# Performance work log

Measured on AMD Instinct MI355X. Metric: run time of the kernel, lower is better.

## Reference

```python
import jax, jax.numpy as jnp
import numpy as np

N = 50000          # total nodes (1000 graphs x 50 agents)
E = 800000         # edges
B = 1000           # batch of graphs -> one agent node each
IN_DIM = 64
HID = 32           # hidden_dim == TransformerConv out_channels per head
HEADS = 4
OUT_DIM = 5
FINAL = HID + HID * HEADS * 2  # 288


def _tconv(x, src, dst, wq, bq, wk, bk, wv, bv):
    """PyG TransformerConv, root_weight=False, concat=True, no edge_attr."""
    n = x.shape[0]
    q = (x @ wq + bq).reshape(n, HEADS, HID)
    k = (x @ wk + bk).reshape(n, HEADS, HID)
    v = (x @ wv + bv).reshape(n, HEADS, HID)
    # per-edge attention logits: query at target, key at source
    alpha = jnp.sum(q[dst] * k[src], axis=-1) / jnp.sqrt(jnp.float32(HID))  # [E, HEADS]
    # segment softmax over incoming edges of each target node
    amax = jax.lax.stop_gradient(jax.ops.segment_max(alpha, dst, num_segments=n))
    ex = jnp.exp(alpha - amax[dst])
    denom = jax.ops.segment_sum(ex, dst, num_segments=n)
    attn = ex / (denom[dst] + 1e-16)                                        # [E, HEADS]
    out = jax.ops.segment_sum(v[src] * attn[..., None], dst, num_segments=n)
    return out.reshape(n, HEADS * HID)


def setup_inputs() -> dict:
    key = jax.random.key(0)
    ks = jax.random.split(key, 24)
    g = lambda i, shape, fan: (jax.random.normal(ks[i], shape, jnp.float32)
                               / jnp.sqrt(jnp.float32(fan)))
    d1 = HID * HEADS  # conv1 output width / conv2 input width
    inp = {
        "x": jax.random.normal(ks[0], (N, IN_DIM), jnp.float32),
        "edge_index": jax.random.randint(ks[1], (2, E), 0, N, jnp.int64),
        "dm_mask": (jax.random.uniform(ks[2], (N, 1)) > 0.5).astype(jnp.float32),
        "global_indices": jax.random.randint(ks[3], (B,), 0, N, jnp.int64),
        # encoder MLP: in -> hid (relu) -> hid
        "enc_w1": g(4, (IN_DIM, HID), IN_DIM), "enc_b1": jnp.zeros((HID,), jnp.float32),
        "enc_w2": g(5, (HID, HID), HID),       "enc_b2": jnp.zeros((HID,), jnp.float32),
        # conv1: hid -> heads*hid
        "c1_wq": g(6, (HID, d1), HID), "c1_bq": jnp.zeros((d1,), jnp.float32),
        "c1_wk": g(7, (HID, d1), HID), "c1_bk": jnp.zeros((d1,), jnp.float32),
        "c1_wv": g(8, (HID, d1), HID), "c1_bv": jnp.zeros((d1,), jnp.float32),
        # conv2: heads*hid -> heads*hid
        "c2_wq": g(9, (d1, d1), d1),  "c2_bq": jnp.zeros((d1,), jnp.float32),
        "c2_wk": g(10, (d1, d1), d1), "c2_bk": jnp.zeros((d1,), jnp.float32),
        "c2_wv": g(11, (d1, d1), d1), "c2_bv": jnp.zeros((d1,), jnp.float32),
        # output head
        "out_w": g(12, (FINAL, OUT_DIM), FINAL),
        "out_b": jnp.zeros((OUT_DIM,), jnp.float32),
    }
    return inp


def reference(x, edge_index, dm_mask, global_indices,
              enc_w1, enc_b1, enc_w2, enc_b2,
              c1_wq, c1_bq, c1_wk, c1_bk, c1_wv, c1_bv,
              c2_wq, c2_bq, c2_wk, c2_bk, c2_wv, c2_bv,
              out_w, out_b):
    src, dst = edge_index[0], edge_index[1]
    # encoder MLP + relu (forward applies F.relu on encoder output)
    h = jax.nn.relu(x @ enc_w1 + enc_b1)
    h = jax.nn.relu(h @ enc_w2 + enc_b2)            # [N, HID]
    x1 = h[global_indices]                          # [B, HID]
    h = jax.nn.relu(_tconv(h, src, dst, c1_wq, c1_bq, c1_wk, c1_bk, c1_wv, c1_bv))
    x2 = h[global_indices]                          # [B, HEADS*HID]
    h = h * dm_mask                                 # decision-maker masking
    h = jax.nn.relu(_tconv(h, src, dst, c2_wq, c2_bq, c2_wk, c2_bk, c2_wv, c2_bv))
    x3 = h[global_indices]                          # [B, HEADS*HID]
    x_cat = jnp.concatenate([x1, x2, x3], axis=1)   # [B, FINAL]
    return x_cat @ out_w + out_b                    # [B, OUT_DIM]
```

## Files before the change

kernel.cpp:

```cpp
#include <hip/hip_runtime.h>
#include <math.h>


typedef _Float16 half8 __attribute__((ext_vector_type(8)));
typedef float f32x4 __attribute__((ext_vector_type(4)));

__device__ inline half8 h8zero() {
    half8 r;
#pragma unroll
    for (int j = 0; j < 8; ++j) r[j] = (_Float16)0.f;
    return r;
}

__device__ __forceinline__ void enc_body(const float* __restrict__ x,
                                         const float* __restrict__ w1, const float* __restrict__ b1,
                                         const float* __restrict__ w2, const float* __restrict__ b2,
                                         _Float16* __restrict__ h0, int n, int bn,
                                         float* __restrict__ smem) {
    float* W1s = smem;
    float* W2s = smem + 2048;
    float* B1s = smem + 3072;
    float* B2s = smem + 3104;
    float* xs  = smem + 3136;
    float* hs  = smem + 3648;
    int t = threadIdx.x;
    for (int i = t; i < 64 * 32; i += 256) W1s[i] = w1[i];
    for (int i = t; i < 32 * 32; i += 256) W2s[i] = w2[i];
    if (t < 32) { B1s[t] = b1[t]; B2s[t] = b2[t]; }
    if (t < 128) {
        int row = t >> 4;
        float4 val = make_float4(0.f, 0.f, 0.f, 0.f);
        if (bn + row < n) val = *(const float4*)(x + (size_t)bn * 64 + t * 4);
        ((float4*)xs)[t] = val;
    }
    __syncthreads();
    int nn = t >> 5, c = t & 31;
    float acc = B1s[c];
#pragma unroll
    for (int i = 0; i < 64; ++i) acc += xs[nn * 64 + i] * W1s[i * 32 + c];
    acc = fmaxf(acc, 0.f);
    hs[nn * 32 + c] = acc;
    __syncthreads();
    float acc2 = B2s[c];
#pragma unroll
    for (int i = 0; i < 32; ++i) acc2 += hs[nn * 32 + i] * W2s[i * 32 + c];
    acc2 = fmaxf(acc2, 0.f);
    int node = bn + nn;
    if (node < n) h0[(size_t)node * 32 + c] = (_Float16)acc2;
}

__global__ __launch_bounds__(256)
void prep_kernel(const float* __restrict__ x,
                 const float* __restrict__ ew1, const float* __restrict__ eb1,
                 const float* __restrict__ ew2, const float* __restrict__ eb2,
                 _Float16* __restrict__ h0,
                 const float* __restrict__ q1, const float* __restrict__ k1,
                 const float* __restrict__ v1, _Float16* __restrict__ WT1,
                 const float* __restrict__ q2, const float* __restrict__ k2,
                 const float* __restrict__ v2, _Float16* __restrict__ WT2,
                 const int* __restrict__ dstv, int* __restrict__ deg, int* __restrict__ eslot,
                 int n, int e, int wtb, int histb) {
    __shared__ float smem[3904];
    int b = blockIdx.x, t = threadIdx.x;
    if (b < wtb) {
        int tid = b * 256 + t;
        const int n1 = 3 * 128 * 32;
        if (tid < n1) {
            int z = tid / (128 * 32);
            int rem = tid % (128 * 32);
            int c = rem / 32, k = rem % 32;
            const float* w = (z == 0) ? q1 : ((z == 1) ? k1 : v1);
            WT1[tid] = (_Float16)w[k * 128 + c];
        } else {
            int i = tid - n1;
            if (i < 3 * 128 * 128) {
                int z = i / (128 * 128);
                int rem = i % (128 * 128);
                int c = rem / 128, k = rem % 128;
                const float* w = (z == 0) ? q2 : ((z == 1) ? k2 : v2);
                WT2[i] = (_Float16)w[k * 128 + c];
            }
        }
    } else if (b < wtb + histb) {
        int i = (b - wtb) * 256 + t;
        if (i < e) eslot[i] = atomicAdd(&deg[dstv[i]], 1);
    } else {
        enc_body(x, ew1, eb1, ew2, eb2, h0, n, (b - wtb - histb) * 8, smem);
    }
}

__device__ __forceinline__ void qkv_body(const _Float16* __restrict__ X, const float* __restrict__ mask,
                                         const _Float16* __restrict__ WT,
                                         const float* __restrict__ Bq, const float* __restrict__ Bk,
                                         const float* __restrict__ Bv,
                                         _Float16* __restrict__ Q, _Float16* __restrict__ KV,
                                         int n, int IN, int bx, int z,
                                         _Float16* __restrict__ Xs, _Float16* __restrict__ Ws) {
    int t = threadIdx.x;
    int bm = bx * 64;
    const float* Bz = (z == 0) ? Bq : ((z == 1) ? Bk : Bv);
    _Float16* Y;
    size_t ystride;
    if (z == 0) { Y = Q; ystride = 128; }
    else        { Y = KV + (z == 1 ? 0 : 128); ystride = 256; }

    int lane = t & 63, w = t >> 6;
    int wr = w >> 1, wc = w & 1;
    int fr = lane & 15, k0 = (lane >> 4) * 8;
    f32x4 acc[2][4];
#pragma unroll
    for (int i = 0; i < 2; ++i)
#pragma unroll
        for (int j = 0; j < 4; ++j)
#pragma unroll
            for (int r = 0; r < 4; ++r) acc[i][j][r] = 0.f;

    int srow = t >> 2, sseg = (t & 3) * 8;
    int snode = bm + srow;
    const _Float16* xbase = X + (size_t)snode * IN + sseg;
    const _Float16* wbase = WT + (size_t)(z * 128) * IN + sseg;
    bool xvalid = (snode < n);
    if (xvalid && mask) xvalid = (mask[snode] != 0.f);

    for (int kt = 0; kt < IN; kt += 32) {
        half8 xv = h8zero();
        if (xvalid) xv = *(const half8*)(xbase + kt);
        half8 wv0 = *(const half8*)(wbase + (size_t)srow * IN + kt);
        half8 wv1 = *(const half8*)(wbase + (size_t)(64 + srow) * IN + kt);
        __syncthreads();
        *(half8*)&Xs[srow * 40 + sseg] = xv;
        *(half8*)&Ws[srow * 40 + sseg] = wv0;
        *(half8*)&Ws[(64 + srow) * 40 + sseg] = wv1;
        __syncthreads();
        half8 a0 = *(const half8*)&Xs[(wr * 32 + fr) * 40 + k0];
        half8 a1 = *(const half8*)&Xs[(wr * 32 + 16 + fr) * 40 + k0];
#pragma unroll
        for (int tc = 0; tc < 4; ++tc) {
            half8 bfr = *(const half8*)&Ws[(wc * 64 + tc * 16 + fr) * 40 + k0];
            acc[0][tc] = __builtin_amdgcn_mfma_f32_16x16x32_f16(a0, bfr, acc[0][tc], 0, 0, 0);
            acc[1][tc] = __builtin_amdgcn_mfma_f32_16x16x32_f16(a1, bfr, acc[1][tc], 0, 0, 0);
        }
    }
#pragma unroll
    for (int tc = 0; tc < 4; ++tc) {
        int colc = wc * 64 + tc * 16 + fr;
        float bias = Bz[colc];
#pragma unroll
        for (int tr = 0; tr < 2; ++tr) {
#pragma unroll
            for (int reg = 0; reg < 4; ++reg) {
                int node = bm + wr * 32 + tr * 16 + (lane >> 4) * 4 + reg;
                if (node < n) Y[(size_t)node * ystride + colc] = (_Float16)(acc[tr][tc][reg] + bias);
            }
        }
    }
}

__global__ __launch_bounds__(256)
void scan1_qkv1_kernel(const int* __restrict__ deg, int* __restrict__ rp,
                       int* __restrict__ bsum, int n, int nb,
                       const _Float16* __restrict__ h0, const _Float16* __restrict__ WT1,
                       const float* __restrict__ bq, const float* __restrict__ bk,
                       const float* __restrict__ bv,
                       _Float16* __restrict__ Q, _Float16* __restrict__ KV, int nqx) {
    __shared__ _Float16 sm[64 * 40 + 128 * 40];
    int b = blockIdx.x;
    if (b < nb) {
        int* s = (int*)sm;
        int t = threadIdx.x;
        int gid = b * 256 + t;
        int v = (gid < n) ? deg[gid] : 0;
        s[t] = v;
        __syncthreads();
#pragma unroll
        for (int off = 1; off < 256; off <<= 1) {
            int tv = (t >= off) ? s[t - off] : 0;
            __syncthreads();
            s[t] += tv;
            __syncthreads();
        }
        if (gid < n) rp[gid] = s[t] - v;
        if (t == 255) bsum[b] = s[255];
    } else {
        int r = b - nb;
        int z = r / nqx, bx = r % nqx;
        qkv_body(h0, nullptr, WT1, bq, bk, bv, Q, KV, n, 32, bx, z, sm, sm + 64 * 40);
    }
}

__global__ __launch_bounds__(256)
void qkv2_kernel(const _Float16* __restrict__ X, const float* __restrict__ mask,
                 const _Float16* __restrict__ WT,
                 const float* __restrict__ Bq, const float* __restrict__ Bk,
                 const float* __restrict__ Bv,
                 _Float16* __restrict__ Q, _Float16* __restrict__ KV, int n, int IN) {
    __shared__ _Float16 Xs[64 * 40];
    __shared__ _Float16 Ws[128 * 40];
    qkv_body(X, mask, WT, Bq, Bk, Bv, Q, KV, n, IN, blockIdx.x, blockIdx.y, Xs, Ws);
}

__global__ void scan2_kernel(int* bsum, int nb) {
    __shared__ int s[256];
    int t = threadIdx.x;
    int v = (t < nb) ? bsum[t] : 0;
    s[t] = v;
    __syncthreads();
#pragma unroll
    for (int off = 1; off < 256; off <<= 1) {
        int tv = (t >= off) ? s[t - off] : 0;
        __syncthreads();
        s[t] += tv;
        __syncthreads();
    }
    if (t < nb) bsum[t] = s[t] - v;
}
__global__ void scan3_kernel(int* rp, const int* __restrict__ bsum, int n) {
    int gid = blockIdx.x * 256 + threadIdx.x;
    if (gid < n) rp[gid] += bsum[blockIdx.x];
}
__global__ void scatter_kernel(const int* __restrict__ src, const int* __restrict__ dst,
                               const int* __restrict__ rp, const int* __restrict__ eslot,
                               int* __restrict__ col, int e) {
    int i = blockIdx.x * 256 + threadIdx.x;
    if (i < e) col[rp[dst[i]] + eslot[i]] = src[i];
}

__global__ __launch_bounds__(256)
void attn_kernel(const _Float16* __restrict__ q, const _Float16* __restrict__ kv,
                 const int* __restrict__ rp, const int* __restrict__ deg,
                 const int* __restrict__ col,
                 _Float16* __restrict__ out, int n) {
    int w = threadIdx.x >> 6;
    int lane = threadIdx.x & 63;
    int node = blockIdx.x * 4 + w;
    if (node >= n) return;
    int es = lane >> 4;
    int l = lane & 15;
    int d0 = l * 8;
    float qf[8];
    {
        half8 qh = *(const half8*)(q + (size_t)node * 128 + d0);
#pragma unroll
        for (int j = 0; j < 8; ++j) qf[j] = (float)qh[j];
    }
    int start = rp[node], len = deg[node];
    float s = 0.f;
    float acc[8];
#pragma unroll
    for (int j = 0; j < 8; ++j) acc[j] = 0.f;
    const float sc = 0.17677669529663689f * 1.4426950408889634f;

    for (int i = es; i < len; i += 4) {
        int srcn = col[start + i];
        const _Float16* row = kv + (size_t)srcn * 256 + d0;
        half8 kf = *(const half8*)row;
        float dot = 0.f;
#pragma unroll
        for (int j = 0; j < 8; ++j) dot += qf[j] * (float)kf[j];
        dot += __shfl_xor(dot, 1);
        dot += __shfl_xor(dot, 2);
        float a = fminf(fmaxf(dot * sc, -120.f), 120.f);
        float p = __builtin_amdgcn_exp2f(a);
        half8 vf = *(const half8*)(row + 128);
        s += p;
#pragma unroll
        for (int j = 0; j < 8; ++j) acc[j] += p * (float)vf[j];
    }
#pragma unroll
    for (int half = 16; half <= 32; half <<= 1) {
        s += __shfl_xor(s, half);
#pragma unroll
        for (int j = 0; j < 8; ++j) acc[j] += __shfl_xor(acc[j], half);
    }
    if (es == 0) {
        float inv = 1.f / (s + 1e-16f);
        half8 r;
#pragma unroll
        for (int j = 0; j < 8; ++j) r[j] = (_Float16)fmaxf(acc[j] * inv, 0.f);
        *(half8*)(out + (size_t)node * 128 + d0) = r;
    }
}

__global__ void head_kernel(const _Float16* __restrict__ h0, const _Float16* __restrict__ h1,
                            const _Float16* __restrict__ h2, const int* __restrict__ gi,
                            const float* __restrict__ ow, const float* __restrict__ ob,
                            float* __restrict__ out, int bsz) {
    int idx = blockIdx.x * 256 + threadIdx.x;
    if (idx >= bsz * 5) return;
    int b = idx / 5, c = idx % 5;
    int g = gi[b];
    float acc = ob[c];
    const _Float16* r0 = h0 + (size_t)g * 32;
#pragma unroll
    for (int i = 0; i < 32; ++i) acc += (float)r0[i] * ow[i * 5 + c];
    const _Float16* r1 = h1 + (size_t)g * 128;
#pragma unroll
    for (int i = 0; i < 128; ++i) acc += (float)r1[i] * ow[(32 + i) * 5 + c];
    const _Float16* r2 = h2 + (size_t)g * 128;
#pragma unroll
    for (int i = 0; i < 128; ++i) acc += (float)r2[i] * ow[(160 + i) * 5 + c];
    out[idx] = acc;
}

extern "C" void kernel_launch(void* const* d_in, const int* in_sizes, int n_in,
                              void* d_out, int out_size, void* d_ws, size_t ws_size,
                              hipStream_t stream) {
    const float* x    = (const float*)d_in[0];
    const int*   ei   = (const int*)d_in[1];
    const float* dm   = (const float*)d_in[2];
    const int*   gi   = (const int*)d_in[3];
    const float* ew1  = (const float*)d_in[4];
    const float* eb1  = (const float*)d_in[5];
    const float* ew2  = (const float*)d_in[6];
    const float* eb2  = (const float*)d_in[7];
    const float* c1wq = (const float*)d_in[8];
    const float* c1bq = (const float*)d_in[9];
    const float* c1wk = (const float*)d_in[10];
    const float* c1bk = (const float*)d_in[11];
    const float* c1wv = (const float*)d_in[12];
    const float* c1bv = (const float*)d_in[13];
    const float* c2wq = (const float*)d_in[14];
    const float* c2bq = (const float*)d_in[15];
    const float* c2wk = (const float*)d_in[16];
    const float* c2bk = (const float*)d_in[17];
    const float* c2wv = (const float*)d_in[18];
    const float* c2bv = (const float*)d_in[19];
    const float* ow   = (const float*)d_in[20];
    const float* ob   = (const float*)d_in[21];
    float* out = (float*)d_out;

    int N = in_sizes[0] / 64;
    int E = in_sizes[1] / 2;
    int B = in_sizes[3];
    const int* srcv = ei;
    const int* dstv = ei + E;

    char* ws = (char*)d_ws;
    size_t off = 0;
    auto alloc = [&](size_t bytes) -> void* {
        void* p = ws + off;
        off += (bytes + 255) & ~(size_t)255;
        return p;
    };
    _Float16* h0   = (_Float16*)alloc((size_t)N * 32 * 2);
    _Float16* h1   = (_Float16*)alloc((size_t)N * 128 * 2);
    _Float16* h2   = (_Float16*)alloc((size_t)N * 128 * 2);
    _Float16* Q    = (_Float16*)alloc((size_t)N * 128 * 2);
    _Float16* KV   = (_Float16*)alloc((size_t)N * 256 * 2);
    _Float16* WT1  = (_Float16*)alloc((size_t)3 * 128 * 32 * 2);
    _Float16* WT2  = (_Float16*)alloc((size_t)3 * 128 * 128 * 2);
    int* deg   = (int*)alloc((size_t)N * 4);
    int* rp    = (int*)alloc((size_t)N * 4);
    int* eslot = (int*)alloc((size_t)E * 4);
    int* colb  = (int*)alloc((size_t)E * 4);
    int* bsum  = (int*)alloc(4096);

    hipMemsetAsync(deg, 0, (size_t)N * 4, stream);

    int eb = (E + 255) / 256;
    int nb = (N + 255) / 256;
    int nqx = (N + 63) / 64;
    int wtb = (3 * 128 * 32 + 3 * 128 * 128 + 255) / 256;

    prep_kernel<<<wtb + eb + (N + 7) / 8, 256, 0, stream>>>(
        x, ew1, eb1, ew2, eb2, h0,
        c1wq, c1wk, c1wv, WT1, c2wq, c2wk, c2wv, WT2,
        dstv, deg, eslot, N, E, wtb, eb);

    scan1_qkv1_kernel<<<nb + 3 * nqx, 256, 0, stream>>>(
        deg, rp, bsum, N, nb, h0, WT1, c1bq, c1bk, c1bv, Q, KV, nqx);

    scan2_kernel<<<1, 256, 0, stream>>>(bsum, nb);
    scan3_kernel<<<nb, 256, 0, stream>>>(rp, bsum, N);
    scatter_kernel<<<eb, 256, 0, stream>>>(srcv, dstv, rp, eslot, colb, E);

    attn_kernel<<<(N + 3) / 4, 256, 0, stream>>>(Q, KV, rp, deg, colb, h1, N);

    dim3 gq(nqx, 3);
    qkv2_kernel<<<gq, 256, 0, stream>>>(h1, dm, WT2, c2bq, c2bk, c2bv, Q, KV, N, 128);
    attn_kernel<<<(N + 3) / 4, 256, 0, stream>>>(Q, KV, rp, deg, colb, h2, N);

    head_kernel<<<(B * 5 + 255) / 256, 256, 0, stream>>>(h0, h1, h2, gi, ow, ob, out, B);
}
```

Baseline: 244.9 us.

## Replace CSR scan with atomic segment allocation and restructure attention edge parallelism

```diff
diff --git a/kernel.cpp b/kernel.cpp
--- a/kernel.cpp
+++ b/kernel.cpp
@@ -3,6 +3,7 @@
 
 
 typedef _Float16 half8 __attribute__((ext_vector_type(8)));
+typedef _Float16 half2t __attribute__((ext_vector_type(2)));
 typedef float f32x4 __attribute__((ext_vector_type(4)));
 
 __device__ inline half8 h8zero() {
@@ -10,6 +11,22 @@
 #pragma unroll
     for (int j = 0; j < 8; ++j) r[j] = (_Float16)0.f;
     return r;
+}
+
+__device__ __forceinline__ float dot8(half8 a, half8 b, float c) {
+#if __has_builtin(__builtin_amdgcn_fdot2)
+#pragma unroll
+    for (int j = 0; j < 4; ++j) {
+        half2t x, y;
+        x[0] = a[2 * j]; x[1] = a[2 * j + 1];
+        y[0] = b[2 * j]; y[1] = b[2 * j + 1];
+        c = __builtin_amdgcn_fdot2(x, y, c, false);
+    }
+#else
+#pragma unroll
+    for (int j = 0; j < 8; ++j) c += (float)a[j] * (float)b[j];
+#endif
+    return c;
 }
 
 __device__ __forceinline__ void enc_body(const float* __restrict__ x,
@@ -157,32 +174,31 @@
 }
 
 __global__ __launch_bounds__(256)
-void scan1_qkv1_kernel(const int* __restrict__ deg, int* __restrict__ rp,
-                       int* __restrict__ bsum, int n, int nb,
+void alloc_qkv1_kernel(const int* __restrict__ deg, int* __restrict__ rp,
+                       int* __restrict__ cnt, int n, int nab,
                        const _Float16* __restrict__ h0, const _Float16* __restrict__ WT1,
                        const float* __restrict__ bq, const float* __restrict__ bk,
                        const float* __restrict__ bv,
                        _Float16* __restrict__ Q, _Float16* __restrict__ KV, int nqx) {
     __shared__ _Float16 sm[64 * 40 + 128 * 40];
     int b = blockIdx.x;
-    if (b < nb) {
-        int* s = (int*)sm;
-        int t = threadIdx.x;
+    if (b < nab) {
+        int t = threadIdx.x, lane = t & 63;
         int gid = b * 256 + t;
         int v = (gid < n) ? deg[gid] : 0;
-        s[t] = v;
-        __syncthreads();
-#pragma unroll
-        for (int off = 1; off < 256; off <<= 1) {
-            int tv = (t >= off) ? s[t - off] : 0;
-            __syncthreads();
-            s[t] += tv;
-            __syncthreads();
-        }
-        if (gid < n) rp[gid] = s[t] - v;
-        if (t == 255) bsum[b] = s[255];
+        int incl = v;
+#pragma unroll
+        for (int off = 1; off < 64; off <<= 1) {
+            int tv = __shfl_up(incl, off);
+            if (lane >= off) incl += tv;
+        }
+        int tot = __shfl(incl, 63);
+        int base = 0;
+        if (lane == 0 && tot > 0) base = atomicAdd(cnt, tot);
+        base = __shfl(base, 0);
+        if (gid < n) rp[gid] = base + incl - v;
     } else {
-        int r = b - nb;
+        int r = b - nab;
         int z = r / nqx, bx = r % nqx;
         qkv_body(h0, nullptr, WT1, bq, bk, bv, Q, KV, n, 32, bx, z, sm, sm + 64 * 40);
     }
@@ -199,25 +215,6 @@
     qkv_body(X, mask, WT, Bq, Bk, Bv, Q, KV, n, IN, blockIdx.x, blockIdx.y, Xs, Ws);
 }
 
-__global__ void scan2_kernel(int* bsum, int nb) {
-    __shared__ int s[256];
-    int t = threadIdx.x;
-    int v = (t < nb) ? bsum[t] : 0;
-    s[t] = v;
-    __syncthreads();
-#pragma unroll
-    for (int off = 1; off < 256; off <<= 1) {
-        int tv = (t >= off) ? s[t - off] : 0;
-        __syncthreads();
-        s[t] += tv;
-        __syncthreads();
-    }
-    if (t < nb) bsum[t] = s[t] - v;
-}
-__global__ void scan3_kernel(int* rp, const int* __restrict__ bsum, int n) {
-    int gid = blockIdx.x * 256 + threadIdx.x;
-    if (gid < n) rp[gid] += bsum[blockIdx.x];
-}
 __global__ void scatter_kernel(const int* __restrict__ src, const int* __restrict__ dst,
                                const int* __restrict__ rp, const int* __restrict__ eslot,
                                int* __restrict__ col, int e) {
@@ -234,15 +231,18 @@
     int lane = threadIdx.x & 63;
     int node = blockIdx.x * 4 + w;
     if (node >= n) return;
-    int es = lane >> 4;
-    int l = lane & 15;
-    int d0 = l * 8;
-    float qf[8];
-    {
-        half8 qh = *(const half8*)(q + (size_t)node * 128 + d0);
-#pragma unroll
-        for (int j = 0; j < 8; ++j) qf[j] = (float)qh[j];
-    }
+    int eo  = lane >> 2;
+    int hq  = lane & 3;
+    int dl  = lane & 15;
+    int sub = lane >> 4;
+    int hd  = dl >> 2;
+
+    const _Float16* qp = q + (size_t)node * 128 + hq * 32;
+    half8 q0 = *(const half8*)(qp);
+    half8 q1 = *(const half8*)(qp + 8);
+    half8 q2 = *(const half8*)(qp + 16);
+    half8 q3 = *(const half8*)(qp + 24);
+
     int start = rp[node], len = deg[node];
     float s = 0.f;
     float acc[8];
@@ -250,34 +250,46 @@
     for (int j = 0; j < 8; ++j) acc[j] = 0.f;
     const float sc = 0.17677669529663689f * 1.4426950408889634f;
 
-    for (int i = es; i < len; i += 4) {
-        int srcn = col[start + i];
-        const _Float16* row = kv + (size_t)srcn * 256 + d0;
-        half8 kf = *(const half8*)row;
+    for (int base = 0; base < len; base += 16) {
+        int rem = len - base;
+        int i = base + eo;
+        bool valid = (i < len);
+        int srcn = valid ? col[start + i] : 0;
+        const _Float16* kp = kv + (size_t)srcn * 256 + hq * 32;
+        half8 k0 = *(const half8*)(kp);
+        half8 k1 = *(const half8*)(kp + 8);
+        half8 k2 = *(const half8*)(kp + 16);
+        half8 k3 = *(const half8*)(kp + 24);
         float dot = 0.f;
-#pragma unroll
-        for (int j = 0; j < 8; ++j) dot += qf[j] * (float)kf[j];
-        dot += __shfl_xor(dot, 1);
-        dot += __shfl_xor(dot, 2);
+        dot = dot8(q0, k0, dot);
+        dot = dot8(q1, k1, dot);
+        dot = dot8(q2, k2, dot);
+        dot = dot8(q3, k3, dot);
         float a = fminf(fmaxf(dot * sc, -120.f), 120.f);
-        float p = __builtin_amdgcn_exp2f(a);
-        half8 vf = *(const half8*)(row + 128);
-        s += p;
-#pragma unroll
-        for (int j = 0; j < 8; ++j) acc[j] += p * (float)vf[j];
-    }
-#pragma unroll
-    for (int half = 16; half <= 32; half <<= 1) {
-        s += __shfl_xor(s, half);
-#pragma unroll
-        for (int j = 0; j < 8; ++j) acc[j] += __shfl_xor(acc[j], half);
-    }
-    if (es == 0) {
+        float p = valid ? __builtin_amdgcn_exp2f(a) : 0.f;
+        int ng = (rem >= 16) ? 4 : ((rem + 3) >> 2);
+        for (int g = 0; g < ng; ++g) {
+            int e = g * 4 + sub;
+            float pj = __shfl(p, e * 4 + hd);
+            int   sj = __shfl(srcn, e * 4);
+            half8 vf = *(const half8*)(kv + (size_t)sj * 256 + 128 + dl * 8);
+            s += pj;
+#pragma unroll
+            for (int j = 0; j < 8; ++j) acc[j] += pj * (float)vf[j];
+        }
+    }
+#pragma unroll
+    for (int mask = 16; mask <= 32; mask <<= 1) {
+        s += __shfl_xor(s, mask);
+#pragma unroll
+        for (int j = 0; j < 8; ++j) acc[j] += __shfl_xor(acc[j], mask);
+    }
+    if (sub == 0) {
         float inv = 1.f / (s + 1e-16f);
         half8 r;
 #pragma unroll
         for (int j = 0; j < 8; ++j) r[j] = (_Float16)fmaxf(acc[j] * inv, 0.f);
-        *(half8*)(out + (size_t)node * 128 + d0) = r;
+        *(half8*)(out + (size_t)node * 128 + dl * 8) = r;
     }
 }
 
@@ -349,16 +361,16 @@
     _Float16* KV   = (_Float16*)alloc((size_t)N * 256 * 2);
     _Float16* WT1  = (_Float16*)alloc((size_t)3 * 128 * 32 * 2);
     _Float16* WT2  = (_Float16*)alloc((size_t)3 * 128 * 128 * 2);
+    int* cnt   = (int*)alloc(256);
     int* deg   = (int*)alloc((size_t)N * 4);
     int* rp    = (int*)alloc((size_t)N * 4);
     int* eslot = (int*)alloc((size_t)E * 4);
     int* colb  = (int*)alloc((size_t)E * 4);
-    int* bsum  = (int*)alloc(4096);
-
-    hipMemsetAsync(deg, 0, (size_t)N * 4, stream);
-
-    int eb = (E + 255) / 256;
-    int nb = (N + 255) / 256;
+
+    hipMemsetAsync(cnt, 0, 256 + (size_t)N * 4, stream);
+
+    int eb  = (E + 255) / 256;
+    int nab = (N + 255) / 256;
     int nqx = (N + 63) / 64;
     int wtb = (3 * 128 * 32 + 3 * 128 * 128 + 255) / 256;
 
@@ -367,11 +379,9 @@
         c1wq, c1wk, c1wv, WT1, c2wq, c2wk, c2wv, WT2,
         dstv, deg, eslot, N, E, wtb, eb);
 
-    scan1_qkv1_kernel<<<nb + 3 * nqx, 256, 0, stream>>>(
-        deg, rp, bsum, N, nb, h0, WT1, c1bq, c1bk, c1bv, Q, KV, nqx);
-
-    scan2_kernel<<<1, 256, 0, stream>>>(bsum, nb);
-    scan3_kernel<<<nb, 256, 0, stream>>>(rp, bsum, N);
+    alloc_qkv1_kernel<<<nab + 3 * nqx, 256, 0, stream>>>(
+        deg, rp, cnt, N, nab, h0, WT1, c1bq, c1bk, c1bv, Q, KV, nqx);
+
     scatter_kernel<<<eb, 256, 0, stream>>>(srcv, dstv, rp, eslot, colb, E);
 
     attn_kernel<<<(N + 3) / 4, 256, 0, stream>>>(Q, KV, rp, deg, colb, h1, N);
```

New measurement: 249.7 us. Within noise of the previous version (+2.0%).
